# Kernel tuning notes

Measured on AMD Instinct MI355X. Metric: run time of the kernel, lower is better.

## Reference

```python
import jax, jax.numpy as jnp
import numpy as np

B, S, H, F, E, K = 2, 2048, 1024, 4096, 8, 2


def setup_inputs() -> dict:
    key = jax.random.key(0)
    ks = jax.random.split(key, 5)
    scale = 0.02
    return {
        "hidden_states": jax.random.normal(ks[0], (B, S, H), jnp.float32),
        "gate_w": jax.random.normal(ks[1], (H, E), jnp.float32) * scale,  # nn.Linear(H,E,bias=False)
        "w1": jax.random.normal(ks[2], (E, H, F), jnp.float32) * scale,   # per-expert fc1
        "b1": jnp.zeros((E, F), jnp.float32),
        "w2": jax.random.normal(ks[3], (E, F, H), jnp.float32) * scale,   # per-expert fc2
        "b2": jnp.zeros((E, H), jnp.float32),
    }


def reference(hidden_states, gate_w, w1, b1, w2, b2):
    b, s, h = hidden_states.shape
    x = hidden_states.reshape(b * s, h)  # [T, H]
    T = x.shape[0]
    n_experts = gate_w.shape[1]

    # --- Top-K gating ---
    router_logits = x @ gate_w                      # [T, E]
    router_probs = jax.nn.softmax(router_logits, axis=-1)
    topk_probs, topk_idx = jax.lax.top_k(router_probs, K)  # [T, K]
    topk_probs = topk_probs / topk_probs.sum(axis=-1, keepdims=True)
    aux_loss = n_experts * jnp.sum(router_probs.mean(axis=0) ** 2)

    # --- Combine weights: scatter normalized top-k probs into dense [T, E] ---
    combine_w = jnp.zeros((T, n_experts), x.dtype).at[
        jnp.arange(T)[:, None], topk_idx
    ].add(topk_probs)

    # --- Expert MLPs (dense per-expert batched GEMM; zero combine weight drops unrouted) ---
    hidden = jax.nn.relu(jnp.einsum('th,ehf->etf', x, w1) + b1[:, None, :])  # [E, T, F]
    expert_out = jnp.einsum('etf,efh->eth', hidden, w2) + b2[:, None, :]     # [E, T, H]

    out = jnp.einsum('te,eth->th', combine_w, expert_out)  # weighted combine
    return out.reshape(b, s, h), aux_loss
```

## Files before the change

### kernel.cpp

```cpp
#include <hip/hip_runtime.h>
#include <hip/hip_bf16.h>
#include <cstdint>

#define AS1 __attribute__((address_space(1)))
#define AS3 __attribute__((address_space(3)))

typedef __attribute__((ext_vector_type(8))) short short8x;
typedef __attribute__((ext_vector_type(4))) float f32x4;

static constexpr int T    = 4096;
static constexpr int HD   = 1024;
static constexpr int FD   = 4096;
static constexpr int NE   = 8;
static constexpr int P    = T * 2;
static constexpr int PPAD = P + 128;
static constexpr int MAXT = P / 128 + NE;
static constexpr int RTB  = 16;
static constexpr int RNB  = T / RTB;

static constexpr int TW1G = (FD / 64) * (HD / 64) * NE;
static constexpr int CVTG = (T * HD) / 1024;
static constexpr int FC1G = (FD / 128) * MAXT;
static constexpr int TW2G = (HD / 64) * (FD / 64) * NE;

struct TileDesc { int e; int start; int rows; int pad; };

__device__ __forceinline__ uint16_t f2bf(float f) {
  uint32_t u = __builtin_bit_cast(uint32_t, f);
  u += 0x7FFFu + ((u >> 16) & 1u);
  return (uint16_t)(u >> 16);
}
__device__ __forceinline__ float bf2f(uint16_t b) {
  uint32_t u = ((uint32_t)b) << 16;
  return __builtin_bit_cast(float, u);
}
__device__ __forceinline__ void gload_lds16(const void* g, void* l) {
  __builtin_amdgcn_global_load_lds((const AS1 uint32_t*)g, (AS3 uint32_t*)l, 16, 0, 0);
}

__device__ __forceinline__ void transpose_role(
    const float* __restrict__ in, uint16_t* __restrict__ out,
    int R, int C, int bi, float* tile ) {
  int nbc = C / 64;
  int nbr = R / 64;
  int cx = bi % nbc;
  int ry = (bi / nbc) % nbr;
  int z  = bi / (nbc * nbr);
  const float* inp = in + (size_t)z * R * C;
  uint16_t* outp = out + (size_t)z * R * C;
  int r0 = ry * 64, c0 = cx * 64;
  int tid = threadIdx.x;
  int lr = tid >> 4;
  int lc4 = (tid & 15) * 4;
#pragma unroll
  for (int p = 0; p < 4; ++p) {
    float4 v = *(const float4*)&inp[(size_t)(r0 + lr + p * 16) * C + c0 + lc4];
    tile[(lr + p * 16) * 65 + lc4 + 0] = v.x;
    tile[(lr + p * 16) * 65 + lc4 + 1] = v.y;
    tile[(lr + p * 16) * 65 + lc4 + 2] = v.z;
    tile[(lr + p * 16) * 65 + lc4 + 3] = v.w;
  }
  __syncthreads();
#pragma unroll
  for (int p = 0; p < 4; ++p) {
    int c = lr + p * 16;
    ushort4 o;
    o.x = f2bf(tile[(lc4 + 0) * 65 + c]);
    o.y = f2bf(tile[(lc4 + 1) * 65 + c]);
    o.z = f2bf(tile[(lc4 + 2) * 65 + c]);
    o.w = f2bf(tile[(lc4 + 3) * 65 + c]);
    *(ushort4*)&outp[(size_t)(c0 + c) * R + r0 + lc4] = o;
  }
}

__device__ __forceinline__ void cvt_role(const float* __restrict__ x,
                                         uint16_t* __restrict__ xb, int bi) {
  size_t i = ((size_t)bi * 256 + threadIdx.x) * 4;
  float4 v = *(const float4*)&x[i];
  ushort4 o;
  o.x = f2bf(v.x); o.y = f2bf(v.y); o.z = f2bf(v.z); o.w = f2bf(v.w);
  *(ushort4*)&xb[i] = o;
}

__device__ __forceinline__ void router_role(
    const float* __restrict__ x, const float* __restrict__ gate_w,
    int* __restrict__ topk_idx, float* __restrict__ topk_w,
    float* __restrict__ part_sums, int* __restrict__ part_counts,
    int rb, char* smem) {
  float* ls = (float*)smem;
  int*   lc = (int*)(smem + 32);
  int tid = threadIdx.x;
  if (tid < NE) { ls[tid] = 0.f; lc[tid] = 0; }
  __syncthreads();
  int wave = tid >> 6, lane = tid & 63;
  float psum[NE];
#pragma unroll
  for (int e = 0; e < NE; ++e) psum[e] = 0.f;

  for (int tt = 0; tt < RTB / 4; ++tt) {
    int t = rb * RTB + wave * (RTB / 4) + tt;
    const float* xr = x + (size_t)t * HD;
    float acc[NE];
#pragma unroll
    for (int e = 0; e < NE; ++e) acc[e] = 0.f;
    for (int i = 0; i < HD / 64; ++i) {
      int h = lane + i * 64;
      float xv = xr[h];
      float4 g0 = *(const float4*)&gate_w[(size_t)h * 8];
      float4 g1 = *(const float4*)&gate_w[(size_t)h * 8 + 4];
      acc[0] += xv * g0.x; acc[1] += xv * g0.y;
      acc[2] += xv * g0.z; acc[3] += xv * g0.w;
      acc[4] += xv * g1.x; acc[5] += xv * g1.y;
      acc[6] += xv * g1.z; acc[7] += xv * g1.w;
    }
#pragma unroll
    for (int off = 32; off > 0; off >>= 1)
#pragma unroll
      for (int e = 0; e < NE; ++e) acc[e] += __shfl_down(acc[e], off);
    if (lane == 0) {
      float m = acc[0];
#pragma unroll
      for (int e = 1; e < NE; ++e) m = fmaxf(m, acc[e]);
      float p[NE], s = 0.f;
#pragma unroll
      for (int e = 0; e < NE; ++e) { p[e] = expf(acc[e] - m); s += p[e]; }
      float inv = 1.f / s;
#pragma unroll
      for (int e = 0; e < NE; ++e) { p[e] *= inv; psum[e] += p[e]; }
      int i0 = 0;
#pragma unroll
      for (int e = 1; e < NE; ++e) if (p[e] > p[i0]) i0 = e;
      int i1 = (i0 == 0) ? 1 : 0;
#pragma unroll
      for (int e = 0; e < NE; ++e) if (e != i0 && e != i1 && p[e] > p[i1]) i1 = e;
      float wsum = p[i0] + p[i1];
      topk_idx[t * 2] = i0; topk_idx[t * 2 + 1] = i1;
      topk_w[t * 2] = p[i0] / wsum; topk_w[t * 2 + 1] = p[i1] / wsum;
      atomicAdd(&lc[i0], 1); atomicAdd(&lc[i1], 1);
    }
  }
  if (lane == 0)
#pragma unroll
    for (int e = 0; e < NE; ++e) atomicAdd(&ls[e], psum[e]);
  __syncthreads();
  if (tid < NE) {
    part_sums[rb * NE + tid]   = ls[tid];
    part_counts[rb * NE + tid] = lc[tid];
  }
}

__global__ __launch_bounds__(256) void prep_kernel(
    const float* __restrict__ x, const float* __restrict__ gate_w,
    const float* __restrict__ w1,
    uint16_t* __restrict__ xb, uint16_t* __restrict__ w1t,
    int* __restrict__ topk_idx, float* __restrict__ topk_w,
    float* __restrict__ part_sums, int* __restrict__ part_counts) {
  __shared__ __align__(16) char smem[16640];
  int b = blockIdx.x;
  if (b < TW1G) {
    transpose_role(w1, w1t, HD, FD, b, (float*)smem);
  } else if (b < TW1G + CVTG) {
    cvt_role(x, xb, b - TW1G);
  } else {
    router_role(x, gate_w, topk_idx, topk_w, part_sums, part_counts,
                b - TW1G - CVTG, smem);
  }
}

__global__ __launch_bounds__(64) void finalize_kernel(
    const int* __restrict__ part_counts, const float* __restrict__ part_sums,
    int* __restrict__ offsets, TileDesc* __restrict__ desc,
    int* __restrict__ ntiles, float* __restrict__ aux_out) {
  __shared__ int   csh[NE];
  __shared__ float ssh[NE];
  int tid = threadIdx.x;
  if (tid < NE) {
    int c = 0; float s = 0.f;
    for (int b = 0; b < RNB; ++b) {
      c += part_counts[b * NE + tid];
      s += part_sums[b * NE + tid];
    }
    csh[tid] = c; ssh[tid] = s;
  }
  __syncthreads();
  if (tid == 0) {
    int off = 0, nt = 0;
    for (int e = 0; e < NE; ++e) {
      offsets[e] = off;
      int c = csh[e];
      for (int i = 0; i < c; i += 128) {
        int rows = c - i; if (rows > 128) rows = 128;
        desc[nt].e = e; desc[nt].start = off + i; desc[nt].rows = rows; desc[nt].pad = 0;
        nt++;
      }
      off += c;
    }
    *ntiles = nt;
    float aux = 0.f;
    for (int e = 0; e < NE; ++e) {
      float mean = ssh[e] / (float)T;
      aux += mean * mean;
    }
    *aux_out = (float)NE * aux;
  }
}

__global__ __launch_bounds__(256) void scatter_kernel(
    const int* __restrict__ topk_idx, const int* __restrict__ offsets,
    int* __restrict__ fill, int* __restrict__ pair_tok, int* __restrict__ tok_pos) {
  int t = blockIdx.x * 256 + threadIdx.x;
  int lane = threadIdx.x & 63;
  unsigned long long below = (lane == 63) ? ~0ull >> 1
                                          : ((1ull << (lane + 1)) - 1) >> 1;
#pragma unroll
  for (int k = 0; k < 2; ++k) {
    int e = topk_idx[t * 2 + k];
    int pos = 0;
    for (int ex = 0; ex < NE; ++ex) {
      unsigned long long m = __ballot(e == ex);
      if (e == ex) {
        int leader = __ffsll((long long)m) - 1;
        int cnt = __popcll(m);
        int base = 0;
        if (lane == leader) base = atomicAdd(&fill[ex], cnt);
        base = __shfl(base, leader);
        pos = base + __popcll(m & below);
      }
    }
    int pp = offsets[e] + pos;
    pair_tok[pp] = t;
    tok_pos[t * 2 + k] = pp;
  }
}

template <int KD, int ND, int NBG, int EPI>
__device__ __forceinline__ void gemm_role(
    char* smem, int orig,
    const uint16_t* __restrict__ Abase, const int* __restrict__ pair_tok,
    const uint16_t* __restrict__ Bw, const float* __restrict__ bias,
    uint16_t* __restrict__ Cout, const TileDesc* __restrict__ desc,
    const int* __restrict__ ntiles) {
  constexpr int SM = MAXT / 8;

  int xcd = orig & 7, local = orig >> 3;
  int nbq = local / (SM * NBG);
  int rem = local % (SM * NBG);
  int mt  = xcd * SM + rem / NBG;
  int nb  = nbq * NBG + rem % NBG;
  if (mt >= *ntiles) return;
  TileDesc d = desc[mt];

  uint16_t* As = (uint16_t*)smem;
  uint16_t* Bs = (uint16_t*)(smem + 8192);
  int* rowA    = (int*)(smem + 16384);

  int tid = threadIdx.x, lane = tid & 63, wave = tid >> 6;
  int wm = wave >> 1, wn = wave & 1;

  int idx0 = (wave * 2 + 0) * 64 + lane;
  int idx1 = (wave * 2 + 1) * 64 + lane;
  int ar0 = idx0 >> 2, kc0 = idx0 & 3;
  int ar1 = idx1 >> 2, kc1 = idx1 & 3;

  int ra0, ra1;
  if constexpr (EPI == 0) {
    if (tid < 128) rowA[tid] = (tid < d.rows) ? pair_tok[d.start + tid] : 0;
    __syncthreads();
    ra0 = rowA[ar0]; ra1 = rowA[ar1];
  } else {
    ra0 = d.start + ar0; ra1 = d.start + ar1;
  }

  const uint16_t* Bbase = Bw + ((size_t)d.e * ND + (size_t)nb * 128) * KD;

  f32x4 acc[4][4];
#pragma unroll
  for (int i = 0; i < 4; ++i)
#pragma unroll
    for (int j = 0; j < 4; ++j) acc[i][j] = (f32x4){0.f, 0.f, 0.f, 0.f};

  for (int kt = 0; kt < KD / 32; ++kt) {
    if (kt) __syncthreads();
    int kb = kt * 32;
    gload_lds16(Abase + (size_t)ra0 * KD + kb + kc0 * 8, &As[(wave * 2 + 0) * 512]);
    gload_lds16(Abase + (size_t)ra1 * KD + kb + kc1 * 8, &As[(wave * 2 + 1) * 512]);
    gload_lds16(Bbase + (size_t)ar0 * KD + kb + kc0 * 8, &Bs[(wave * 2 + 0) * 512]);
    gload_lds16(Bbase + (size_t)ar1 * KD + kb + kc1 * 8, &Bs[(wave * 2 + 1) * 512]);
    __syncthreads();

    short8x af[4], bfr[4];
#pragma unroll
    for (int i = 0; i < 4; ++i)
      af[i] = *(const short8x*)&As[(wm * 64 + i * 16 + (lane & 15)) * 32 + (lane >> 4) * 8];
#pragma unroll
    for (int j = 0; j < 4; ++j)
      bfr[j] = *(const short8x*)&Bs[(wn * 64 + j * 16 + (lane & 15)) * 32 + (lane >> 4) * 8];
#pragma unroll
    for (int i = 0; i < 4; ++i)
#pragma unroll
      for (int j = 0; j < 4; ++j)
        acc[i][j] = __builtin_amdgcn_mfma_f32_16x16x32_bf16(af[i], bfr[j], acc[i][j], 0, 0, 0);
  }

  int rq = (lane >> 4) * 4;
  int cl = lane & 15;
#pragma unroll
  for (int i = 0; i < 4; ++i) {
    int rb = wm * 64 + i * 16 + rq;
#pragma unroll
    for (int j = 0; j < 4; ++j) {
      int col = nb * 128 + wn * 64 + j * 16 + cl;
      float bv = bias[d.e * ND + col];
#pragma unroll
      for (int q = 0; q < 4; ++q) {
        int r = rb + q;
        if (r < d.rows) {
          float v = acc[i][j][q] + bv;
          if (EPI == 0) v = fmaxf(v, 0.f);
          Cout[(size_t)(d.start + r) * ND + col] = f2bf(v);
        }
      }
    }
  }
}

__global__ __launch_bounds__(256) void fc1_fused_kernel(
    const uint16_t* __restrict__ xb, const int* __restrict__ pair_tok,
    const uint16_t* __restrict__ w1t, const float* __restrict__ b1,
    uint16_t* __restrict__ hidden, const TileDesc* __restrict__ desc,
    const int* __restrict__ ntiles,
    const float* __restrict__ w2, uint16_t* __restrict__ w2t) {
  __shared__ __align__(16) char smem[17408];
  int b = blockIdx.x;
  if (b < FC1G) {
    gemm_role<HD, FD, 4, 0>(smem, b, xb, pair_tok, w1t, b1, hidden, desc, ntiles);
  } else {
    transpose_role(w2, w2t, FD, HD, b - FC1G, (float*)smem);
  }
}

__global__ __launch_bounds__(256) void fc2_kernel(
    const uint16_t* __restrict__ hidden, const uint16_t* __restrict__ w2t,
    const float* __restrict__ b2, uint16_t* __restrict__ pout,
    const TileDesc* __restrict__ desc, const int* __restrict__ ntiles) {
  __shared__ __align__(16) char smem[17408];
  gemm_role<FD, HD, 8, 1>(smem, blockIdx.x, hidden, nullptr, w2t, b2, pout, desc, ntiles);
}

__global__ __launch_bounds__(256) void combine_kernel(
    const uint16_t* __restrict__ po, const int* __restrict__ tok_pos,
    const float* __restrict__ topk_w, float* __restrict__ out) {
  int t = blockIdx.x;
  int c = threadIdx.x * 4;
  int p0 = tok_pos[t * 2], p1 = tok_pos[t * 2 + 1];
  float w0 = topk_w[t * 2], w1 = topk_w[t * 2 + 1];
  ushort4 a = *(const ushort4*)&po[(size_t)p0 * HD + c];
  ushort4 b = *(const ushort4*)&po[(size_t)p1 * HD + c];
  float4 o;
  o.x = w0 * bf2f(a.x) + w1 * bf2f(b.x);
  o.y = w0 * bf2f(a.y) + w1 * bf2f(b.y);
  o.z = w0 * bf2f(a.z) + w1 * bf2f(b.z);
  o.w = w0 * bf2f(a.w) + w1 * bf2f(b.w);
  *(float4*)&out[(size_t)t * HD + c] = o;
}

extern "C" void kernel_launch(void* const* d_in, const int* in_sizes, int n_in,
                              void* d_out, int out_size, void* d_ws, size_t ws_size,
                              hipStream_t stream) {
  const float* x      = (const float*)d_in[0];
  const float* gate_w = (const float*)d_in[1];
  const float* w1     = (const float*)d_in[2];
  const float* b1     = (const float*)d_in[3];
  const float* w2     = (const float*)d_in[4];
  const float* b2     = (const float*)d_in[5];
  float* out = (float*)d_out;
  (void)in_sizes; (void)n_in; (void)out_size; (void)ws_size;

  char* w = (char*)d_ws;
  size_t off = 0;
  auto alloc = [&](size_t bytes) -> void* {
    void* p = w + off;
    off = (off + bytes + 255) & ~(size_t)255;
    return p;
  };
  int*      meta     = (int*)alloc(256);
  int*      fill     = meta;
  int*      offsets  = (int*)alloc(256);
  int*      ntiles   = offsets + 8;
  TileDesc* desc     = (TileDesc*)alloc(sizeof(TileDesc) * 128);
  int*      topk_idx = (int*)alloc(sizeof(int) * P);
  float*    topk_w   = (float*)alloc(sizeof(float) * P);
  int*      tok_pos  = (int*)alloc(sizeof(int) * P);
  int*      pair_tok = (int*)alloc(sizeof(int) * PPAD);
  float*    psums    = (float*)alloc(sizeof(float) * RNB * NE);
  int*      pcounts  = (int*)alloc(sizeof(int) * RNB * NE);
  uint16_t* xb       = (uint16_t*)alloc((size_t)T * HD * 2);
  uint16_t* w1t      = (uint16_t*)alloc((size_t)NE * FD * HD * 2);
  uint16_t* w2t      = (uint16_t*)alloc((size_t)NE * HD * FD * 2);
  uint16_t* hidden   = (uint16_t*)alloc((size_t)PPAD * FD * 2);
  uint16_t* pout     = (uint16_t*)alloc((size_t)PPAD * HD * 2);

  hipMemsetAsync(meta, 0, 256, stream);
  prep_kernel<<<TW1G + CVTG + RNB, 256, 0, stream>>>(
      x, gate_w, w1, xb, w1t, topk_idx, topk_w, psums, pcounts);
  finalize_kernel<<<1, 64, 0, stream>>>(pcounts, psums, offsets, desc, ntiles,
                                        out + (size_t)T * HD);
  scatter_kernel<<<T / 256, 256, 0, stream>>>(topk_idx, offsets, fill, pair_tok, tok_pos);
  fc1_fused_kernel<<<FC1G + TW2G, 256, 0, stream>>>(
      xb, pair_tok, w1t, b1, hidden, desc, ntiles, w2, w2t);
  fc2_kernel<<<(HD / 128) * MAXT, 256, 0, stream>>>(
      hidden, w2t, b2, pout, desc, ntiles);
  combine_kernel<<<T, 256, 0, stream>>>(pout, tok_pos, topk_w, out);
}
```

Baseline: 386.0 us.

## Use 256-row M tiles for fc1 grouped GEMM with separate tile descriptors

Adds a dedicated fc1 GEMM path that uses 256x128 output tiles, with 8x4 MFMA accumulators per wave, in place of 128x128. The finalize kernel now builds a second descriptor list at 256-row granularity for it, while fc2 keeps the 128-row tiles. The larger tile reuses each B weight tile across twice as many gathered token rows, which halves the weight reloads and cuts block count. The cost is more registers and LDS per block (lower occupancy) and more padding waste on partial expert tiles.

New measurement: 493.6 us. 27.9% more time.

```diff
diff --git a/kernel.cpp b/kernel.cpp
--- a/kernel.cpp
+++ b/kernel.cpp
@@ -13,14 +13,15 @@
 static constexpr int FD   = 4096;
 static constexpr int NE   = 8;
 static constexpr int P    = T * 2;
-static constexpr int PPAD = P + 128;
-static constexpr int MAXT = P / 128 + NE;
+static constexpr int PPAD = P + 256;
+static constexpr int MAXT    = P / 128 + NE;
+static constexpr int MAXT256 = P / 256 + NE;
 static constexpr int RTB  = 16;
 static constexpr int RNB  = T / RTB;
 
 static constexpr int TW1G = (FD / 64) * (HD / 64) * NE;
 static constexpr int CVTG = (T * HD) / 1024;
-static constexpr int FC1G = (FD / 128) * MAXT;
+static constexpr int FC1G = (FD / 128) * MAXT256;
 static constexpr int TW2G = (HD / 64) * (FD / 64) * NE;
 
 struct TileDesc { int e; int start; int rows; int pad; };
@@ -169,8 +170,8 @@
 
 __global__ __launch_bounds__(64) void finalize_kernel(
     const int* __restrict__ part_counts, const float* __restrict__ part_sums,
-    int* __restrict__ offsets, TileDesc* __restrict__ desc,
-    int* __restrict__ ntiles, float* __restrict__ aux_out) {
+    int* __restrict__ offsets, TileDesc* __restrict__ desc128, TileDesc* __restrict__ desc256,
+    int* __restrict__ ntiles128, int* __restrict__ ntiles256, float* __restrict__ aux_out) {
   __shared__ int   csh[NE];
   __shared__ float ssh[NE];
   int tid = threadIdx.x;
@@ -184,18 +185,24 @@
   }
   __syncthreads();
   if (tid == 0) {
-    int off = 0, nt = 0;
+    int off = 0, n1 = 0, n2 = 0;
     for (int e = 0; e < NE; ++e) {
       offsets[e] = off;
       int c = csh[e];
       for (int i = 0; i < c; i += 128) {
         int rows = c - i; if (rows > 128) rows = 128;
-        desc[nt].e = e; desc[nt].start = off + i; desc[nt].rows = rows; desc[nt].pad = 0;
-        nt++;
+        desc128[n1].e = e; desc128[n1].start = off + i; desc128[n1].rows = rows;
+        desc128[n1].pad = 0; n1++;
+      }
+      for (int i = 0; i < c; i += 256) {
+        int rows = c - i; if (rows > 256) rows = 256;
+        desc256[n2].e = e; desc256[n2].start = off + i; desc256[n2].rows = rows;
+        desc256[n2].pad = 0; n2++;
       }
       off += c;
     }
-    *ntiles = nt;
+    *ntiles128 = n1;
+    *ntiles256 = n2;
     float aux = 0.f;
     for (int e = 0; e < NE; ++e) {
       float mean = ssh[e] / (float)T;
@@ -233,13 +240,105 @@
   }
 }
 
-template <int KD, int ND, int NBG, int EPI>
-__device__ __forceinline__ void gemm_role(
+__device__ __forceinline__ void gemm256_role(
     char* smem, int orig,
     const uint16_t* __restrict__ Abase, const int* __restrict__ pair_tok,
     const uint16_t* __restrict__ Bw, const float* __restrict__ bias,
+    uint16_t* __restrict__ Cout, const TileDesc* __restrict__ desc256,
+    const int* __restrict__ nt256) {
+  constexpr int KD = HD;
+  constexpr int ND = FD;
+  constexpr int NBG = 4;
+  constexpr int SM = MAXT256 / 8;
+
+  int xcd = orig & 7, local = orig >> 3;
+  int nbq = local / (SM * NBG);
+  int rem = local % (SM * NBG);
+  int mt  = xcd * SM + rem / NBG;
+  int nb  = nbq * NBG + rem % NBG;
+  if (mt >= *nt256) return;
+  TileDesc d = desc256[mt];
+
+  uint16_t* As = (uint16_t*)smem;
+  uint16_t* Bs = (uint16_t*)(smem + 16384);
+  int* rowA    = (int*)(smem + 24576);
+
+  int tid = threadIdx.x, lane = tid & 63, wave = tid >> 6;
+  int wm = wave >> 1, wn = wave & 1;
+  int l15 = lane & 15, lk = lane >> 4;
+
+  if (tid < 256) rowA[tid] = (tid < d.rows) ? pair_tok[d.start + tid] : 0;
+  __syncthreads();
+
+  int srow = tid >> 2, skc = (tid & 3) * 8;
+  const uint16_t* Asrc[4];
+  const uint16_t* Bsrc[2];
+#pragma unroll
+  for (int i = 0; i < 4; ++i)
+    Asrc[i] = Abase + (size_t)rowA[i * 64 + srow] * KD + skc;
+#pragma unroll
+  for (int j = 0; j < 2; ++j)
+    Bsrc[j] = Bw + ((size_t)d.e * ND + (size_t)nb * 128 + j * 64 + srow) * KD + skc;
+
+  f32x4 acc[8][4];
+#pragma unroll
+  for (int i = 0; i < 8; ++i)
+#pragma unroll
+    for (int j = 0; j < 4; ++j) acc[i][j] = (f32x4){0.f, 0.f, 0.f, 0.f};
+
+  for (int kt = 0; kt < KD / 32; ++kt) {
+    if (kt) __syncthreads();
+    int kb = kt * 32;
+#pragma unroll
+    for (int i = 0; i < 4; ++i)
+      gload_lds16(Asrc[i] + kb, &As[i * 2048 + tid * 8]);
+#pragma unroll
+    for (int j = 0; j < 2; ++j)
+      gload_lds16(Bsrc[j] + kb, &Bs[j * 2048 + tid * 8]);
+    __syncthreads();
+
+    short8x bfr[4];
+#pragma unroll
+    for (int j = 0; j < 4; ++j)
+      bfr[j] = *(const short8x*)&Bs[(wn * 64 + j * 16 + l15) * 32 + lk * 8];
+#pragma unroll
+    for (int f = 0; f < 8; ++f) {
+      short8x af = *(const short8x*)&As[(wm * 128 + f * 16 + l15) * 32 + lk * 8];
+#pragma unroll
+      for (int j = 0; j < 4; ++j)
+        acc[f][j] = __builtin_amdgcn_mfma_f32_16x16x32_bf16(af, bfr[j], acc[f][j], 0, 0, 0);
+    }
+  }
+
+  int rq = lk * 4, cl = l15;
+#pragma unroll
+  for (int f = 0; f < 8; ++f) {
+    int rb = wm * 128 + f * 16 + rq;
+#pragma unroll
+    for (int j = 0; j < 4; ++j) {
+      int col = nb * 128 + wn * 64 + j * 16 + cl;
+      float bv = bias[d.e * ND + col];
+#pragma unroll
+      for (int q = 0; q < 4; ++q) {
+        int r = rb + q;
+        if (r < d.rows) {
+          float v = fmaxf(acc[f][j][q] + bv, 0.f);
+          Cout[(size_t)(d.start + r) * ND + col] = f2bf(v);
+        }
+      }
+    }
+  }
+}
+
+__device__ __forceinline__ void gemm_role(
+    char* smem, int orig,
+    const uint16_t* __restrict__ Abase,
+    const uint16_t* __restrict__ Bw, const float* __restrict__ bias,
     uint16_t* __restrict__ Cout, const TileDesc* __restrict__ desc,
     const int* __restrict__ ntiles) {
+  constexpr int KD = FD;
+  constexpr int ND = HD;
+  constexpr int NBG = 8;
   constexpr int SM = MAXT / 8;
 
   int xcd = orig & 7, local = orig >> 3;
@@ -252,7 +351,6 @@
 
   uint16_t* As = (uint16_t*)smem;
   uint16_t* Bs = (uint16_t*)(smem + 8192);
-  int* rowA    = (int*)(smem + 16384);
 
   int tid = threadIdx.x, lane = tid & 63, wave = tid >> 6;
   int wm = wave >> 1, wn = wave & 1;
@@ -261,15 +359,7 @@
   int idx1 = (wave * 2 + 1) * 64 + lane;
   int ar0 = idx0 >> 2, kc0 = idx0 & 3;
   int ar1 = idx1 >> 2, kc1 = idx1 & 3;
-
-  int ra0, ra1;
-  if constexpr (EPI == 0) {
-    if (tid < 128) rowA[tid] = (tid < d.rows) ? pair_tok[d.start + tid] : 0;
-    __syncthreads();
-    ra0 = rowA[ar0]; ra1 = rowA[ar1];
-  } else {
-    ra0 = d.start + ar0; ra1 = d.start + ar1;
-  }
+  int ra0 = d.start + ar0, ra1 = d.start + ar1;
 
   const uint16_t* Bbase = Bw + ((size_t)d.e * ND + (size_t)nb * 128) * KD;
 
@@ -315,9 +405,7 @@
       for (int q = 0; q < 4; ++q) {
         int r = rb + q;
         if (r < d.rows) {
-          float v = acc[i][j][q] + bv;
-          if (EPI == 0) v = fmaxf(v, 0.f);
-          Cout[(size_t)(d.start + r) * ND + col] = f2bf(v);
+          Cout[(size_t)(d.start + r) * ND + col] = f2bf(acc[i][j][q] + bv);
         }
       }
     }
@@ -327,13 +415,13 @@
 __global__ __launch_bounds__(256) void fc1_fused_kernel(
     const uint16_t* __restrict__ xb, const int* __restrict__ pair_tok,
     const uint16_t* __restrict__ w1t, const float* __restrict__ b1,
-    uint16_t* __restrict__ hidden, const TileDesc* __restrict__ desc,
-    const int* __restrict__ ntiles,
+    uint16_t* __restrict__ hidden, const TileDesc* __restrict__ desc256,
+    const int* __restrict__ nt256,
     const float* __restrict__ w2, uint16_t* __restrict__ w2t) {
-  __shared__ __align__(16) char smem[17408];
+  __shared__ __align__(16) char smem[25856];
   int b = blockIdx.x;
   if (b < FC1G) {
-    gemm_role<HD, FD, 4, 0>(smem, b, xb, pair_tok, w1t, b1, hidden, desc, ntiles);
+    gemm256_role(smem, b, xb, pair_tok, w1t, b1, hidden, desc256, nt256);
   } else {
     transpose_role(w2, w2t, FD, HD, b - FC1G, (float*)smem);
   }
@@ -342,9 +430,9 @@
 __global__ __launch_bounds__(256) void fc2_kernel(
     const uint16_t* __restrict__ hidden, const uint16_t* __restrict__ w2t,
     const float* __restrict__ b2, uint16_t* __restrict__ pout,
-    const TileDesc* __restrict__ desc, const int* __restrict__ ntiles) {
-  __shared__ __align__(16) char smem[17408];
-  gemm_role<FD, HD, 8, 1>(smem, blockIdx.x, hidden, nullptr, w2t, b2, pout, desc, ntiles);
+    const TileDesc* __restrict__ desc128, const int* __restrict__ nt128) {
+  __shared__ __align__(16) char smem[16896];
+  gemm_role(smem, blockIdx.x, hidden, w2t, b2, pout, desc128, nt128);
 }
 
 __global__ __launch_bounds__(256) void combine_kernel(
@@ -383,32 +471,34 @@
     off = (off + bytes + 255) & ~(size_t)255;
     return p;
   };
-  int*      meta     = (int*)alloc(256);
-  int*      fill     = meta;
-  int*      offsets  = (int*)alloc(256);
-  int*      ntiles   = offsets + 8;
-  TileDesc* desc     = (TileDesc*)alloc(sizeof(TileDesc) * 128);
-  int*      topk_idx = (int*)alloc(sizeof(int) * P);
-  float*    topk_w   = (float*)alloc(sizeof(float) * P);
-  int*      tok_pos  = (int*)alloc(sizeof(int) * P);
-  int*      pair_tok = (int*)alloc(sizeof(int) * PPAD);
-  float*    psums    = (float*)alloc(sizeof(float) * RNB * NE);
-  int*      pcounts  = (int*)alloc(sizeof(int) * RNB * NE);
-  uint16_t* xb       = (uint16_t*)alloc((size_t)T * HD * 2);
-  uint16_t* w1t      = (uint16_t*)alloc((size_t)NE * FD * HD * 2);
-  uint16_t* w2t      = (uint16_t*)alloc((size_t)NE * HD * FD * 2);
-  uint16_t* hidden   = (uint16_t*)alloc((size_t)PPAD * FD * 2);
-  uint16_t* pout     = (uint16_t*)alloc((size_t)PPAD * HD * 2);
+  int*      meta      = (int*)alloc(256);
+  int*      fill      = meta;
+  int*      offsets   = (int*)alloc(256);
+  int*      ntiles128 = offsets + 8;
+  int*      ntiles256 = offsets + 9;
+  TileDesc* desc128   = (TileDesc*)alloc(sizeof(TileDesc) * 128);
+  TileDesc* desc256   = (TileDesc*)alloc(sizeof(TileDesc) * 64);
+  int*      topk_idx  = (int*)alloc(sizeof(int) * P);
+  float*    topk_w    = (float*)alloc(sizeof(float) * P);
+  int*      tok_pos   = (int*)alloc(sizeof(int) * P);
+  int*      pair_tok  = (int*)alloc(sizeof(int) * PPAD);
+  float*    psums     = (float*)alloc(sizeof(float) * RNB * NE);
+  int*      pcounts   = (int*)alloc(sizeof(int) * RNB * NE);
+  uint16_t* xb        = (uint16_t*)alloc((size_t)T * HD * 2);
+  uint16_t* w1t       = (uint16_t*)alloc((size_t)NE * FD * HD * 2);
+  uint16_t* w2t       = (uint16_t*)alloc((size_t)NE * HD * FD * 2);
+  uint16_t* hidden    = (uint16_t*)alloc((size_t)PPAD * FD * 2);
+  uint16_t* pout      = (uint16_t*)alloc((size_t)PPAD * HD * 2);
 
   hipMemsetAsync(meta, 0, 256, stream);
   prep_kernel<<<TW1G + CVTG + RNB, 256, 0, stream>>>(
       x, gate_w, w1, xb, w1t, topk_idx, topk_w, psums, pcounts);
-  finalize_kernel<<<1, 64, 0, stream>>>(pcounts, psums, offsets, desc, ntiles,
-                                        out + (size_t)T * HD);
+  finalize_kernel<<<1, 64, 0, stream>>>(pcounts, psums, offsets, desc128, desc256,
+                                        ntiles128, ntiles256, out + (size_t)T * HD);
   scatter_kernel<<<T / 256, 256, 0, stream>>>(topk_idx, offsets, fill, pair_tok, tok_pos);
   fc1_fused_kernel<<<FC1G + TW2G, 256, 0, stream>>>(
-      xb, pair_tok, w1t, b1, hidden, desc, ntiles, w2, w2t);
+      xb, pair_tok, w1t, b1, hidden, desc256, ntiles256, w2, w2t);
   fc2_kernel<<<(HD / 128) * MAXT, 256, 0, stream>>>(
-      hidden, w2t, b2, pout, desc, ntiles);
+      hidden, w2t, b2, pout, desc128, ntiles128);
   combine_kernel<<<T, 256, 0, stream>>>(pout, tok_pos, topk_w, out);
 }
```
